# Kernel optimization log

Hardware: AMD Instinct MI355X
Metric: run time of the kernel (lower is better)

The kernel has to match this reference:

```python
import jax, jax.numpy as jnp
import numpy as np
from jax import lax

GRAVITY = 9.8
DT = 0.1
MAX_STEPS = 200


def _conv(x, w, b):
    # x: [N,C,H,W], w: [O,I,3,3] (PyTorch OIHW), padding=1 -> SAME
    y = lax.conv_general_dilated(x, w, window_strides=(1, 1), padding='SAME',
                                 dimension_numbers=('NCHW', 'OIHW', 'NCHW'))
    return y + b[None, :, None, None]


def _maxpool2(x):
    return lax.reduce_window(x, -jnp.inf, lax.max,
                             window_dimensions=(1, 1, 2, 2),
                             window_strides=(1, 1, 2, 2), padding='VALID')


def setup_inputs() -> dict:
    key = jax.random.key(0)
    ks = jax.random.split(key, 12)
    B = 256
    x = jax.random.normal(ks[0], (B, 12, 128, 128), dtype=jnp.float32)

    def he(k, shape, fan_in):
        return jax.random.normal(k, shape, dtype=jnp.float32) * np.float32(np.sqrt(2.0 / fan_in))

    w1 = he(ks[1], (32, 12, 3, 3), 12 * 9); b1 = jnp.zeros((32,), jnp.float32)
    w2 = he(ks[2], (64, 32, 3, 3), 32 * 9); b2 = jnp.zeros((64,), jnp.float32)
    w3 = he(ks[3], (64, 64, 3, 3), 64 * 9); b3 = jnp.zeros((64,), jnp.float32)
    w4 = he(ks[4], (64, 64, 3, 3), 64 * 9); b4 = jnp.zeros((64,), jnp.float32)
    wl1 = he(ks[5], (128, 64 * 8 * 8), 64 * 8 * 8); bl1 = jnp.zeros((128,), jnp.float32)
    wl2 = he(ks[6], (4, 128), 128); bl2 = jnp.zeros((4,), jnp.float32)
    return {'x': x, 'w1': w1, 'b1': b1, 'w2': w2, 'b2': b2, 'w3': w3, 'b3': b3,
            'w4': w4, 'b4': b4, 'wl1': wl1, 'bl1': bl1, 'wl2': wl2, 'bl2': bl2}


def _forward(x, w1, b1, w2, b2, w3, b3, w4, b4, wl1, bl1, wl2, bl2):
    h = _maxpool2(jax.nn.relu(_conv(x, w1, b1)))   # [B,32,64,64]
    h = _maxpool2(jax.nn.relu(_conv(h, w2, b2)))   # [B,64,32,32]
    h = _maxpool2(jax.nn.relu(_conv(h, w3, b3)))   # [B,64,16,16]
    h = _maxpool2(jax.nn.relu(_conv(h, w4, b4)))   # [B,64,8,8]
    h = h.reshape(h.shape[0], -1)                  # [B,4096]
    h = jax.nn.relu(h @ wl1.T + bl1)               # [B,128]
    state = h @ wl2.T + bl2                        # [B,4]

    px, py, vx, vy = state[:, 0], state[:, 1], state[:, 2], state[:, 3]

    def step(carry, _):
        cx, cy, cvy = carry
        nvy = cvy - GRAVITY * DT
        nx = cx + vx * DT
        ny = jnp.maximum(cy + nvy * DT, 0.0)
        return (nx, ny, nvy), None

    (fx, _, _), _ = lax.scan(step, (px, py, vy), None, length=MAX_STEPS)
    return fx


def reference(x, w1, b1, w2, b2, w3, b3, w4, b4, wl1, bl1, wl2, bl2):
    return _forward(x, w1, b1, w2, b2, w3, b3, w4, b4, wl1, bl1, wl2, bl2)
```

## Files before the change

kernel.cpp:

```cpp
#include <hip/hip_runtime.h>


typedef _Float16 f16;
typedef _Float16 f16x8 __attribute__((ext_vector_type(8)));
typedef _Float16 f16x4 __attribute__((ext_vector_type(4)));
typedef float f32x4 __attribute__((ext_vector_type(4)));
typedef float f32x16 __attribute__((ext_vector_type(16)));

__global__ __launch_bounds__(512)
void pack_weights(const float* __restrict__ w1, const float* __restrict__ w2,
                  const float* __restrict__ w3, const float* __restrict__ w4,
                  f16* __restrict__ apack) {
  int idx = blockIdx.x * 512 + threadIdx.x;
  int frag = idx >> 9;
  int e = idx & 511;
  int lane = e >> 3, j = e & 7;
  float v = 0.f;
  if (frag < 9) {
    int kh = frag / 3, kw = frag % 3;
    int oc = lane & 31;
    int ic = (lane >> 5) * 8 + j;
    if (ic < 12) v = w1[((oc * 12 + ic) * 3 + kh) * 3 + kw];
  } else if (frag < 45) {
    int f = frag - 9;
    int ocg = f & 1;
    int sk = f >> 1;
    int ks = sk & 1, sh = sk >> 1;
    int kh = sh / 3, kw = sh % 3;
    int oc = ocg * 32 + (lane & 31);
    int ic = ks * 16 + (lane >> 5) * 8 + j;
    v = w2[((oc * 32 + ic) * 3 + kh) * 3 + kw];
  } else if (frag < 117) {
    int f = frag - 45;
    int ocg = f & 1;
    int sk = f >> 1;
    int ks = sk & 3, sh = sk >> 2;
    int kh = sh / 3, kw = sh % 3;
    int oc = ocg * 32 + (lane & 31);
    int ic = ks * 16 + (lane >> 5) * 8 + j;
    v = w3[((oc * 64 + ic) * 3 + kh) * 3 + kw];
  } else {
    int f = frag - 117;
    int sk = f >> 2, og = f & 3;
    int sh = sk >> 1, ks = sk & 1;
    int kh = sh / 3, kw = sh % 3;
    int row16 = lane & 15, kg = lane >> 4;
    int oc = og * 16 + row16;
    int ic = ks * 32 + kg * 8 + j;
    v = w4[((oc * 64 + ic) * 3 + kh) * 3 + kw];
  }
  apack[idx] = (f16)v;
}

__global__ __launch_bounds__(512)
void conv1_mfma(const float* __restrict__ x, const f16* __restrict__ apack,
                const float* __restrict__ bias, f16* __restrict__ hout) {
  constexpr int W = 128, H = 128;
  constexpr int PADB = 48, ROWB = 130 * PADB;
  constexpr int TPB = 8;
  __shared__ char smem[6 * ROWB];
  const int tid = threadIdx.x;
  const int n = blockIdx.y;
  const int R0 = blockIdx.x * (TPB * 4);

  if (tid < 36) {
    int slot = tid / 6, r = tid % 6;
    int px = (r >= 3) ? 129 : 0;
    int ch = r % 3;
    *(float4*)(smem + slot * ROWB + px * PADB + ch * 16) =
        make_float4(0.f, 0.f, 0.f, 0.f);
  }

  const int g = tid >> 4;
  const int l16 = tid & 15;
  const int Q = l16 >> 2, q = l16 & 3;

  auto load_row = [&](int ri) -> float4 {
    float4 v = make_float4(0.f, 0.f, 0.f, 0.f);
    if (l16 < 12 && ri >= 0 && ri < H)
      v = *(const float4*)(x + ((size_t)(n * 12 + l16) * H + ri) * W + g * 4);
    return v;
  };
  auto xpose_write = [&](float4 av, int slot) {
    float4 t1, t2;
    {
      float sx = __shfl_xor(av.x, 1), sy = __shfl_xor(av.y, 1);
      float sz = __shfl_xor(av.z, 1), sw = __shfl_xor(av.w, 1);
      bool odd = q & 1;
      t1.x = odd ? sy : av.x;  t1.y = odd ? av.y : sx;
      t1.z = odd ? sw : av.z;  t1.w = odd ? av.w : sz;
    }
    {
      float sx = __shfl_xor(t1.x, 2), sy = __shfl_xor(t1.y, 2);
      float sz = __shfl_xor(t1.z, 2), sw = __shfl_xor(t1.w, 2);
      bool hi2 = q & 2;
      t2.x = hi2 ? sz : t1.x;  t2.y = hi2 ? sw : t1.y;
      t2.z = hi2 ? t1.z : sx;  t2.w = hi2 ? t1.w : sy;
    }
    f16x4 h = { (f16)t2.x, (f16)t2.y, (f16)t2.z, (f16)t2.w };
    *(f16x4*)(smem + slot * ROWB + (g * 4 + q + 1) * PADB + Q * 8) = h;
  };

  const int wv = tid >> 6, l = tid & 63;
  const int rp = wv >> 2;
  const int pxb = (wv & 3) * 32;
  const int rl0 = rp * 2;
  const int ln = l & 31;
  const int hi = l >> 5;

  f16x8 A[9];
#pragma unroll
  for (int ks = 0; ks < 9; ++ks)
    A[ks] = *(const f16x8*)(apack + ((ks << 9) + (l << 3)));

  float4 a[6];
#pragma unroll
  for (int i = 0; i < 6; ++i) a[i] = load_row(R0 - 1 + i);
#pragma unroll
  for (int i = 0; i < 6; ++i) xpose_write(a[i], i);
  __syncthreads();

  int s0 = 0;
  for (int t = 0; t < TPB; ++t) {
    if (t + 1 < TPB) {
#pragma unroll
      for (int i = 0; i < 4; ++i) a[i] = load_row(R0 + 4 * t + 5 + i);
    }
    f32x16 acc0 = (f32x16)0.f, acc1 = (f32x16)0.f;
#pragma unroll
    for (int kw = 0; kw < 3; ++kw) {
      const char* bcol = smem + (pxb + ln + kw) * PADB + hi * 16;
      f16x8 R[4];
#pragma unroll
      for (int j = 0; j < 4; ++j) {
        int sl = s0 + rl0 + j; if (sl >= 6) sl -= 6;
        R[j] = *(const f16x8*)(bcol + sl * ROWB);
      }
#pragma unroll
      for (int kh = 0; kh < 3; ++kh) {
        acc0 = __builtin_amdgcn_mfma_f32_32x32x16_f16(A[kh * 3 + kw], R[kh],     acc0, 0, 0, 0);
        acc1 = __builtin_amdgcn_mfma_f32_32x32x16_f16(A[kh * 3 + kw], R[kh + 1], acc1, 0, 0, 0);
      }
    }
    {
      const int pr = (R0 >> 1) + 2 * t + rp;
#pragma unroll
      for (int gg = 0; gg < 4; ++gg) {
        float v[4];
#pragma unroll
        for (int c = 0; c < 4; ++c) {
          float m = fmaxf(acc0[gg * 4 + c], acc1[gg * 4 + c]);
          v[c] = fmaxf(m, __shfl_xor(m, 1));
        }
        if ((l & 1) == 0) {
          const int pw = (pxb + ln) >> 1;
          const int oc0 = gg * 8 + hi * 4;
          f16x4 pk;
#pragma unroll
          for (int c = 0; c < 4; ++c)
            pk[c] = (f16)fmaxf(v[c] + bias[oc0 + c], 0.f);
          *(f16x4*)(hout + (((size_t)(n * 64 + pr) * 64 + pw) * 32 + oc0)) = pk;
        }
      }
    }
    __syncthreads();
    if (t + 1 < TPB) {
#pragma unroll
      for (int i = 0; i < 4; ++i) {
        int sl = s0 + i; if (sl >= 6) sl -= 6;
        xpose_write(a[i], sl);
      }
      __syncthreads();
    }
    s0 += 4; if (s0 >= 6) s0 -= 6;
  }
}

template<int C, int W, int H, int BR, int PADB>
__global__ __launch_bounds__(256)
void conv_shift32(const f16* __restrict__ hin, const f16* __restrict__ apack,
                  const float* __restrict__ bias, f16* __restrict__ hout) {
  constexpr int KS16 = C / 16;
  constexpr int SR = BR + 2;
  constexpr int ROWB = (W + 2) * PADB;
  __shared__ char smem[SR * ROWB];
  const int tid = threadIdx.x;
  const int n = blockIdx.y;
  const int r0 = blockIdx.x * BR;
  constexpr int CPC = C / 8;
  constexpr int TOTC = SR * (W + 2) * CPC;
  constexpr int NITER = (TOTC + 255) / 256;
  {
    float4 stg[NITER];
#pragma unroll
    for (int it = 0; it < NITER; ++it) {
      const int t = tid + it * 256;
      float4 v = make_float4(0.f, 0.f, 0.f, 0.f);
      if (t < TOTC) {
        int sr = t / ((W + 2) * CPC);
        int rem = t - sr * ((W + 2) * CPC);
        int px = rem / CPC;
        int kc = rem - px * CPC;
        int ri = r0 + sr - 1;
        int gx = px - 1;
        if (ri >= 0 && ri < H && gx >= 0 && gx < W)
          v = *(const float4*)(hin + (((size_t)(n * H + ri) * W + gx) * C + kc * 8));
      }
      stg[it] = v;
    }
#pragma unroll
    for (int it = 0; it < NITER; ++it) {
      const int t = tid + it * 256;
      if (t < TOTC) {
        int sr = t / ((W + 2) * CPC);
        int rem = t - sr * ((W + 2) * CPC);
        int px = rem / CPC;
        int kc = rem - px * CPC;
        *(float4*)(smem + sr * ROWB + px * PADB + kc * 16) = stg[it];
      }
    }
  }
  __syncthreads();

  const int wv = tid >> 6, l = tid & 63;
  constexpr int WPP = W / 32;
  const int rp = wv / WPP;
  const int pxb = (wv % WPP) * 32;
  const int rl0 = rp * 2;
  const int ln = l & 31;
  const int hi = l >> 5;
  const int px0 = pxb + ln;

  f32x16 acc[2][2];
  acc[0][0] = (f32x16)0.f; acc[0][1] = (f32x16)0.f;
  acc[1][0] = (f32x16)0.f; acc[1][1] = (f32x16)0.f;

#pragma unroll
  for (int sh = 0; sh < 9; ++sh) {
    const int kh = sh / 3, kw = sh % 3;
    f16x8 A[KS16][2];
#pragma unroll
    for (int ks = 0; ks < KS16; ++ks)
#pragma unroll
      for (int ocg = 0; ocg < 2; ++ocg)
        A[ks][ocg] = *(const f16x8*)(apack + ((((sh * KS16 + ks) * 2 + ocg) << 9) + (l << 3)));
#pragma unroll
    for (int rowi = 0; rowi < 2; ++rowi) {
      const char* base = smem + (rl0 + rowi + kh) * ROWB + (px0 + kw) * PADB + hi * 16;
#pragma unroll
      for (int ks = 0; ks < KS16; ++ks) {
        f16x8 B = *(const f16x8*)(base + ks * 32);
        acc[rowi][0] = __builtin_amdgcn_mfma_f32_32x32x16_f16(A[ks][0], B, acc[rowi][0], 0, 0, 0);
        acc[rowi][1] = __builtin_amdgcn_mfma_f32_32x32x16_f16(A[ks][1], B, acc[rowi][1], 0, 0, 0);
      }
    }
  }
  constexpr int PH = H / 2, PW = W / 2;
  const int pr = blockIdx.x * (BR / 2) + rp;
#pragma unroll
  for (int ocg = 0; ocg < 2; ++ocg) {
#pragma unroll
    for (int gg = 0; gg < 4; ++gg) {
      float v[4];
#pragma unroll
      for (int c = 0; c < 4; ++c) {
        float m = fmaxf(acc[0][ocg][gg * 4 + c], acc[1][ocg][gg * 4 + c]);
        v[c] = fmaxf(m, __shfl_xor(m, 1));
      }
      if ((l & 1) == 0) {
        const int pw = (pxb + ln) >> 1;
        const int oc0 = ocg * 32 + gg * 8 + hi * 4;
        f16x4 pk;
#pragma unroll
        for (int c = 0; c < 4; ++c)
          pk[c] = (f16)fmaxf(v[c] + bias[oc0 + c], 0.f);
        *(f16x4*)(hout + (((size_t)(n * PH + pr) * PW + pw) * 64 + oc0)) = pk;
      }
    }
  }
}

template<int C, int W, int H, int BR, int KS, int PADB, int PGn, bool NCHW_OUT>
__global__ __launch_bounds__(256)
void conv_shift(const f16* __restrict__ hin, const f16* __restrict__ apack,
                const float* __restrict__ bias, void* __restrict__ hout) {
  constexpr int SR = BR + 2;
  constexpr int ROWB = (W + 2) * PADB;
  __shared__ char smem[SR * ROWB];
  const int tid = threadIdx.x;
  const int n = blockIdx.y;
  const int r0 = blockIdx.x * BR;
  constexpr int CPC = C / 8;
  constexpr int TOTC = SR * (W + 2) * CPC;
  constexpr int NITER = (TOTC + 255) / 256;
  {
    float4 stg[NITER];
#pragma unroll
    for (int it = 0; it < NITER; ++it) {
      const int t = tid + it * 256;
      float4 v = make_float4(0.f, 0.f, 0.f, 0.f);
      if (t < TOTC) {
        int sr = t / ((W + 2) * CPC);
        int rem = t - sr * ((W + 2) * CPC);
        int px = rem / CPC;
        int kc = rem - px * CPC;
        int ri = r0 + sr - 1;
        int gx = px - 1;
        if (ri >= 0 && ri < H && gx >= 0 && gx < W)
          v = *(const float4*)(hin + (((size_t)(n * H + ri) * W + gx) * C + kc * 8));
      }
      stg[it] = v;
    }
#pragma unroll
    for (int it = 0; it < NITER; ++it) {
      const int t = tid + it * 256;
      if (t < TOTC) {
        int sr = t / ((W + 2) * CPC);
        int rem = t - sr * ((W + 2) * CPC);
        int px = rem / CPC;
        int kc = rem - px * CPC;
        *(float4*)(smem + sr * ROWB + px * PADB + kc * 16) = stg[it];
      }
    }
  }
  __syncthreads();

  const int wv = tid >> 6, l = tid & 63;
  constexpr int WPP = W / (16 * PGn);
  const int rp = wv / WPP;
  const int pxb = (wv % WPP) * 16 * PGn;
  const int rl0 = rp * 2;
  const int lp = l & 15, kg = l >> 4;
  const int px0 = pxb + lp;

  f32x4 acc[2][PGn][4];
#pragma unroll
  for (int a = 0; a < 2; ++a)
#pragma unroll
    for (int b = 0; b < PGn; ++b)
#pragma unroll
      for (int c = 0; c < 4; ++c)
        acc[a][b][c] = (f32x4){0.f, 0.f, 0.f, 0.f};

#pragma unroll
  for (int sh = 0; sh < 9; ++sh) {
    const int kh = sh / 3, kw = sh % 3;
    f16x8 A[KS][4];
#pragma unroll
    for (int ks = 0; ks < KS; ++ks)
#pragma unroll
      for (int og = 0; og < 4; ++og)
        A[ks][og] = *(const f16x8*)(apack + ((((sh * KS + ks) * 4 + og) << 9) + (l << 3)));
#pragma unroll
    for (int rowi = 0; rowi < 2; ++rowi) {
      const char* base = smem + (rl0 + rowi + kh) * ROWB;
#pragma unroll
      for (int pg = 0; pg < PGn; ++pg) {
#pragma unroll
        for (int ks = 0; ks < KS; ++ks) {
          f16x8 B = *(const f16x8*)(base + (px0 + pg * 16 + kw) * PADB + ks * 64 + kg * 16);
#pragma unroll
          for (int og = 0; og < 4; ++og)
            acc[rowi][pg][og] =
                __builtin_amdgcn_mfma_f32_16x16x32_f16(A[ks][og], B, acc[rowi][pg][og], 0, 0, 0);
        }
      }
    }
  }
  constexpr int PH = H / 2, PW = W / 2;
  const int pr = blockIdx.x * (BR / 2) + rp;
#pragma unroll
  for (int pg = 0; pg < PGn; ++pg) {
#pragma unroll
    for (int og = 0; og < 4; ++og) {
      float v[4];
#pragma unroll
      for (int c = 0; c < 4; ++c) {
        float m = fmaxf(acc[0][pg][og][c], acc[1][pg][og][c]);
        v[c] = fmaxf(m, __shfl_xor(m, 1));
      }
      if ((l & 1) == 0) {
        const int pw = (pxb + pg * 16 + lp) >> 1;
        const int oc0 = og * 16 + kg * 4;
        if constexpr (NCHW_OUT) {
          float* o = (float*)hout;
#pragma unroll
          for (int c = 0; c < 4; ++c)
            o[(((size_t)n * 64 + oc0 + c) * PH + pr) * PW + pw] =
                fmaxf(v[c] + bias[oc0 + c], 0.f);
        } else {
          f16x4 pk;
#pragma unroll
          for (int c = 0; c < 4; ++c)
            pk[c] = (f16)fmaxf(v[c] + bias[oc0 + c], 0.f);
          *(f16x4*)((f16*)hout + (((size_t)(n * PH + pr) * PW + pw) * 64 + oc0)) = pk;
        }
      }
    }
  }
}

__global__ __launch_bounds__(1024)
void fc_head(const float* __restrict__ h4, const float* __restrict__ wl1,
             const float* __restrict__ bl1, const float* __restrict__ wl2,
             const float* __restrict__ bl2, float* __restrict__ out) {
  __shared__ float rows[2][4096];
  __shared__ float red[8 * 128 * 2];
  __shared__ float red2[2 * 128];
  const int tid = threadIdx.x;
  const int b0 = blockIdx.x * 2;
  {
    const float4* src = (const float4*)(h4 + (size_t)b0 * 4096);
    float4* dst = (float4*)rows;
    for (int t = tid; t < 2048; t += 1024) dst[t] = src[t];
  }
  __syncthreads();

  const int nn = tid & 127;
  const int ks = tid >> 7;
  const float4* wp = (const float4*)(wl1 + (size_t)nn * 4096 + ks * 512);
  const float4* x0 = (const float4*)(&rows[0][ks * 512]);
  const float4* x1 = (const float4*)(&rows[1][ks * 512]);
  float s0 = 0.f, s1 = 0.f;
#pragma unroll 8
  for (int i = 0; i < 128; ++i) {
    float4 w = wp[i], a = x0[i], b = x1[i];
    s0 = fmaf(w.x, a.x, fmaf(w.y, a.y, fmaf(w.z, a.z, fmaf(w.w, a.w, s0))));
    s1 = fmaf(w.x, b.x, fmaf(w.y, b.y, fmaf(w.z, b.z, fmaf(w.w, b.w, s1))));
  }
  red[(ks * 128 + nn) * 2 + 0] = s0;
  red[(ks * 128 + nn) * 2 + 1] = s1;
  __syncthreads();

  if (tid < 256) {
    const int r = tid >> 7, n2 = tid & 127;
    float h = bl1[n2];
#pragma unroll
    for (int k = 0; k < 8; ++k) h += red[(k * 128 + n2) * 2 + r];
    h = fmaxf(h, 0.f);
    red2[r * 128 + n2] = h * (wl2[n2] + 20.0f * wl2[256 + n2]);
  }
  __syncthreads();
#pragma unroll
  for (int s = 64; s > 0; s >>= 1) {
    if (tid < 2 * s) {
      int r = tid / s, i = tid - r * s;
      red2[r * 128 + i] += red2[r * 128 + i + s];
    }
    __syncthreads();
  }
  if (tid < 2) out[b0 + tid] = red2[tid * 128] + bl2[0] + 20.0f * bl2[2];
}

extern "C" void kernel_launch(void* const* d_in, const int* in_sizes, int n_in,
                              void* d_out, int out_size, void* d_ws, size_t ws_size,
                              hipStream_t stream) {
  const float* x   = (const float*)d_in[0];
  const float* w1  = (const float*)d_in[1];
  const float* b1  = (const float*)d_in[2];
  const float* w2  = (const float*)d_in[3];
  const float* b2  = (const float*)d_in[4];
  const float* w3  = (const float*)d_in[5];
  const float* b3  = (const float*)d_in[6];
  const float* w4  = (const float*)d_in[7];
  const float* b4  = (const float*)d_in[8];
  const float* wl1 = (const float*)d_in[9];
  const float* bl1 = (const float*)d_in[10];
  const float* wl2 = (const float*)d_in[11];
  const float* bl2 = (const float*)d_in[12];
  float* out = (float*)d_out;
  char* ws = (char*)d_ws;

  f16* apack = (f16*)ws;
  f16* h1 = (f16*)(ws + (1u << 20));
  f16* h2 = (f16*)(ws + 68157440u);
  f16* h3 = (f16*)(ws + 101711872u);
  float* h4 = (float*)(ws + 110100480u);

  pack_weights<<<189, 512, 0, stream>>>(w1, w2, w3, w4, apack);
  conv1_mfma<<<dim3(4, 256), 512, 0, stream>>>(x, apack, b1, h1);
  conv_shift32<32, 64, 64, 4, 80><<<dim3(16, 256), 256, 0, stream>>>(
      h1, apack + 9 * 512, b2, h2);
  conv_shift32<64, 32, 32, 8, 144><<<dim3(4, 256), 256, 0, stream>>>(
      h2, apack + 45 * 512, b3, h3);
  conv_shift<64, 16, 16, 8, 2, 144, 1, true><<<dim3(2, 256), 256, 0, stream>>>(
      h3, apack + 117 * 512, b4, (void*)h4);
  fc_head<<<128, 1024, 0, stream>>>(h4, wl1, bl1, wl2, bl2, out);
}
```

Measured before the change: 232.6 us.

## Add rolling-buffer conv2 kernel and fp16 FC1 weights

Replaces the conv2 launch with a new kernel in which each block walks 16 rows through a 6-slot shared-memory ring buffer. The next 4 input rows are prefetched into registers while the MFMAs run on the current rows. This cuts halo re-reads and the block count compared with the 4-row-per-block shift kernel. Separately, the FC1 weights are converted to fp16 by a new pack kernel so fc_head reads half the bytes. The cost is one extra launch and slightly lower precision on the FC weights.

```diff
diff --git a/kernel.cpp b/kernel.cpp
--- a/kernel.cpp
+++ b/kernel.cpp
@@ -52,6 +52,14 @@
   apack[idx] = (f16)v;
 }
 
+__global__ __launch_bounds__(256)
+void pack_wl1(const float* __restrict__ wl1, f16* __restrict__ wl1h) {
+  int i = (blockIdx.x * 256 + threadIdx.x) * 4;
+  float4 v = *(const float4*)(wl1 + i);
+  f16x4 h = { (f16)v.x, (f16)v.y, (f16)v.z, (f16)v.w };
+  *(f16x4*)(wl1h + i) = h;
+}
+
 __global__ __launch_bounds__(512)
 void conv1_mfma(const float* __restrict__ x, const f16* __restrict__ apack,
                 const float* __restrict__ bias, f16* __restrict__ hout) {
@@ -173,6 +181,127 @@
       __syncthreads();
     }
     s0 += 4; if (s0 >= 6) s0 -= 6;
+  }
+}
+
+__global__ __launch_bounds__(256)
+void conv2_roll(const f16* __restrict__ hin, const f16* __restrict__ apack,
+                const float* __restrict__ bias, f16* __restrict__ hout) {
+  constexpr int C = 32, W = 64, H = 64;
+  constexpr int PADB = 80, ROWB = 66 * PADB;
+  constexpr int TPB = 4;
+  __shared__ char smem[6 * ROWB];
+  const int tid = threadIdx.x;
+  const int n = blockIdx.y;
+  const int R0 = blockIdx.x * (TPB * 4);
+
+  auto chunk_ld = [&](int c, int rbase) -> float4 {
+    int rowl = c / 264, rem = c - rowl * 264;
+    int px = rem >> 2, kc = rem & 3;
+    int ri = rbase + rowl, gx = px - 1;
+    float4 v = make_float4(0.f, 0.f, 0.f, 0.f);
+    if (ri >= 0 && ri < H && gx >= 0 && gx < W)
+      v = *(const float4*)(hin + (((size_t)(n * H + ri) * W + gx) * C + kc * 8));
+    return v;
+  };
+  auto chunk_st = [&](int c, int sbase, float4 v) {
+    int rowl = c / 264, rem = c - rowl * 264;
+    int px = rem >> 2, kc = rem & 3;
+    int slot = sbase + rowl; if (slot >= 6) slot -= 6;
+    *(float4*)(smem + slot * ROWB + px * PADB + kc * 16) = v;
+  };
+
+  {
+    float4 a[7];
+#pragma unroll
+    for (int it = 0; it < 7; ++it) {
+      int c = tid + it * 256;
+      a[it] = (c < 1584) ? chunk_ld(c, R0 - 1) : make_float4(0.f, 0.f, 0.f, 0.f);
+    }
+#pragma unroll
+    for (int it = 0; it < 7; ++it) {
+      int c = tid + it * 256;
+      if (c < 1584) chunk_st(c, 0, a[it]);
+    }
+  }
+  __syncthreads();
+
+  const int wv = tid >> 6, l = tid & 63;
+  const int rp = wv >> 1;
+  const int pxb = (wv & 1) * 32;
+  const int rl0 = rp * 2;
+  const int ln = l & 31;
+  const int hi = l >> 5;
+
+  float4 a[5];
+  int s04 = 0;
+  for (int t = 0; t < TPB; ++t) {
+    if (t + 1 < TPB) {
+#pragma unroll
+      for (int it = 0; it < 5; ++it) {
+        int c = tid + it * 256;
+        a[it] = (c < 1056) ? chunk_ld(c, R0 + 4 * t + 5)
+                           : make_float4(0.f, 0.f, 0.f, 0.f);
+      }
+    }
+    f32x16 acc[2][2];
+    acc[0][0] = (f32x16)0.f; acc[0][1] = (f32x16)0.f;
+    acc[1][0] = (f32x16)0.f; acc[1][1] = (f32x16)0.f;
+#pragma unroll
+    for (int sh = 0; sh < 9; ++sh) {
+      const int kh = sh / 3, kw = sh % 3;
+      f16x8 A[2][2];
+#pragma unroll
+      for (int ks = 0; ks < 2; ++ks)
+#pragma unroll
+        for (int ocg = 0; ocg < 2; ++ocg)
+          A[ks][ocg] = *(const f16x8*)(apack + ((((sh * 2 + ks) * 2 + ocg) << 9) + (l << 3)));
+#pragma unroll
+      for (int rowi = 0; rowi < 2; ++rowi) {
+        int sl = s04 + rl0 + rowi + kh; if (sl >= 6) sl -= 6;
+        const char* base = smem + sl * ROWB + (pxb + ln + kw) * PADB + hi * 16;
+#pragma unroll
+        for (int ks = 0; ks < 2; ++ks) {
+          f16x8 B = *(const f16x8*)(base + ks * 32);
+          acc[rowi][0] = __builtin_amdgcn_mfma_f32_32x32x16_f16(A[ks][0], B, acc[rowi][0], 0, 0, 0);
+          acc[rowi][1] = __builtin_amdgcn_mfma_f32_32x32x16_f16(A[ks][1], B, acc[rowi][1], 0, 0, 0);
+        }
+      }
+    }
+    {
+      const int pr = (R0 >> 1) + 2 * t + rp;
+#pragma unroll
+      for (int ocg = 0; ocg < 2; ++ocg) {
+#pragma unroll
+        for (int gg = 0; gg < 4; ++gg) {
+          float v[4];
+#pragma unroll
+          for (int c = 0; c < 4; ++c) {
+            float m = fmaxf(acc[0][ocg][gg * 4 + c], acc[1][ocg][gg * 4 + c]);
+            v[c] = fmaxf(m, __shfl_xor(m, 1));
+          }
+          if ((l & 1) == 0) {
+            const int pw = (pxb + ln) >> 1;
+            const int oc0 = ocg * 32 + gg * 8 + hi * 4;
+            f16x4 pk;
+#pragma unroll
+            for (int c = 0; c < 4; ++c)
+              pk[c] = (f16)fmaxf(v[c] + bias[oc0 + c], 0.f);
+            *(f16x4*)(hout + (((size_t)(n * 32 + pr) * 32 + pw) * 64 + oc0)) = pk;
+          }
+        }
+      }
+    }
+    __syncthreads();
+    if (t + 1 < TPB) {
+#pragma unroll
+      for (int it = 0; it < 5; ++it) {
+        int c = tid + it * 256;
+        if (c < 1056) chunk_st(c, s04, a[it]);
+      }
+      __syncthreads();
+    }
+    s04 += 4; if (s04 >= 6) s04 -= 6;
   }
 }
 
@@ -401,7 +530,7 @@
 }
 
 __global__ __launch_bounds__(1024)
-void fc_head(const float* __restrict__ h4, const float* __restrict__ wl1,
+void fc_head(const float* __restrict__ h4, const f16* __restrict__ wl1h,
              const float* __restrict__ bl1, const float* __restrict__ wl2,
              const float* __restrict__ bl2, float* __restrict__ out) {
   __shared__ float rows[2][4096];
@@ -418,15 +547,21 @@
 
   const int nn = tid & 127;
   const int ks = tid >> 7;
-  const float4* wp = (const float4*)(wl1 + (size_t)nn * 4096 + ks * 512);
+  const f16x8* wp = (const f16x8*)(wl1h + (size_t)nn * 4096 + ks * 512);
   const float4* x0 = (const float4*)(&rows[0][ks * 512]);
   const float4* x1 = (const float4*)(&rows[1][ks * 512]);
   float s0 = 0.f, s1 = 0.f;
-#pragma unroll 8
-  for (int i = 0; i < 128; ++i) {
-    float4 w = wp[i], a = x0[i], b = x1[i];
-    s0 = fmaf(w.x, a.x, fmaf(w.y, a.y, fmaf(w.z, a.z, fmaf(w.w, a.w, s0))));
-    s1 = fmaf(w.x, b.x, fmaf(w.y, b.y, fmaf(w.z, b.z, fmaf(w.w, b.w, s1))));
+#pragma unroll 4
+  for (int i = 0; i < 64; ++i) {
+    f16x8 w8 = wp[i];
+    float4 a0 = x0[2 * i], a1 = x0[2 * i + 1];
+    float4 b0 = x1[2 * i], b1 = x1[2 * i + 1];
+    float w0 = (float)w8[0], w1 = (float)w8[1], w2 = (float)w8[2], w3 = (float)w8[3];
+    float w4 = (float)w8[4], w5 = (float)w8[5], w6 = (float)w8[6], w7 = (float)w8[7];
+    s0 = fmaf(w0, a0.x, fmaf(w1, a0.y, fmaf(w2, a0.z, fmaf(w3, a0.w, s0))));
+    s0 = fmaf(w4, a1.x, fmaf(w5, a1.y, fmaf(w6, a1.z, fmaf(w7, a1.w, s0))));
+    s1 = fmaf(w0, b0.x, fmaf(w1, b0.y, fmaf(w2, b0.z, fmaf(w3, b0.w, s1))));
+    s1 = fmaf(w4, b1.x, fmaf(w5, b1.y, fmaf(w6, b1.z, fmaf(w7, b1.w, s1))));
   }
   red[(ks * 128 + nn) * 2 + 0] = s0;
   red[(ks * 128 + nn) * 2 + 1] = s1;
@@ -472,18 +607,19 @@
   char* ws = (char*)d_ws;
 
   f16* apack = (f16*)ws;
-  f16* h1 = (f16*)(ws + (1u << 20));
-  f16* h2 = (f16*)(ws + 68157440u);
-  f16* h3 = (f16*)(ws + 101711872u);
-  float* h4 = (float*)(ws + 110100480u);
+  f16* wl1h  = (f16*)(ws + 524288u);
+  f16* h1 = (f16*)(ws + 2097152u);
+  f16* h2 = (f16*)(ws + 69206016u);
+  f16* h3 = (f16*)(ws + 102760448u);
+  float* h4 = (float*)(ws + 111149056u);
 
   pack_weights<<<189, 512, 0, stream>>>(w1, w2, w3, w4, apack);
+  pack_wl1<<<512, 256, 0, stream>>>(wl1, wl1h);
   conv1_mfma<<<dim3(4, 256), 512, 0, stream>>>(x, apack, b1, h1);
-  conv_shift32<32, 64, 64, 4, 80><<<dim3(16, 256), 256, 0, stream>>>(
-      h1, apack + 9 * 512, b2, h2);
+  conv2_roll<<<dim3(4, 256), 256, 0, stream>>>(h1, apack + 9 * 512, b2, h2);
   conv_shift32<64, 32, 32, 8, 144><<<dim3(4, 256), 256, 0, stream>>>(
       h2, apack + 45 * 512, b3, h3);
   conv_shift<64, 16, 16, 8, 2, 144, 1, true><<<dim3(2, 256), 256, 0, stream>>>(
       h3, apack + 117 * 512, b4, (void*)h4);
-  fc_head<<<128, 1024, 0, stream>>>(h4, wl1, bl1, wl2, bl2, out);
-}
+  fc_head<<<128, 1024, 0, stream>>>(h4, wl1h, bl1, wl2, bl2, out);
+}
```

Result: no change. 233.3 us (+0.3%).
